# Kernel optimization log

Measured on AMD Instinct MI355X. Metric: run time of the kernel, lower is better.

Reference implementation:

```python
import jax, jax.numpy as jnp
import numpy as np

VOCAB, CTX, EMBED, HEADS = 32000, 2048, 1024, 16


def setup_inputs() -> dict:
    key = jax.random.key(0)
    ks = jax.random.split(key, 10)
    E = EMBED
    s = 0.02
    return {
        "x": jax.random.randint(ks[0], (2, 2048), 0, VOCAB, dtype=jnp.int32),
        "tok_emb": jax.random.normal(ks[1], (VOCAB, E), jnp.float32) * s,
        "pos_emb": jax.random.normal(ks[2], (CTX, E), jnp.float32) * s,
        "qkv_w": jax.random.normal(ks[3], (E, 3 * E), jnp.float32) * s,
        "qkv_b": jnp.zeros((3 * E,), jnp.float32),
        "proj_w": jax.random.normal(ks[4], (E, E), jnp.float32) * s,
        "proj_b": jnp.zeros((E,), jnp.float32),
        "fc_w": jax.random.normal(ks[5], (E, VOCAB), jnp.float32) * s,
        "fc_b": jnp.zeros((VOCAB,), jnp.float32),
    }


def reference(x, tok_emb, pos_emb, qkv_w, qkv_b, proj_w, proj_b, fc_w, fc_b):
    B, T = x.shape
    H = HEADS
    E = tok_emb.shape[1]
    hd = E // H
    h = tok_emb[x] + pos_emb[:T][None, :, :]                      # [B,T,E]
    qkv = h @ qkv_w + qkv_b                                       # [B,T,3E]
    q, k, v = jnp.split(qkv, 3, axis=-1)
    # [B,T,E] -> [B,H,T,hd]
    q = q.reshape(B, T, H, hd).transpose(0, 2, 1, 3)
    k = k.reshape(B, T, H, hd).transpose(0, 2, 1, 3)
    v = v.reshape(B, T, H, hd).transpose(0, 2, 1, 3)
    att = jnp.einsum("bhqd,bhkd->bhqk", q, k) / jnp.sqrt(jnp.float32(hd))
    causal = jnp.tril(jnp.ones((T, T), dtype=bool))
    att = jnp.where(causal[None, None], att, jnp.float32(-jnp.inf))
    att = jax.nn.softmax(att, axis=-1)
    out = jnp.einsum("bhqk,bhkd->bhqd", att, v)                   # [B,H,T,hd]
    out = out.transpose(0, 2, 1, 3).reshape(B, T, E)
    out = out @ proj_w + proj_b
    return out @ fc_w + fc_b                                      # [B,T,VOCAB]
```

## Files before the change

### kernel.cpp

```cpp
#include <hip/hip_runtime.h>

#define BATCH 2
#define T 2048
#define E 1024
#define NH 16
#define HD 64
#define M (BATCH*T)
#define K3 (3*E)
#define VOCAB 32000

typedef __attribute__((ext_vector_type(8))) short s16x8;
typedef __attribute__((ext_vector_type(4))) short s16x4;
typedef __attribute__((ext_vector_type(4))) float f32x4;

__device__ inline unsigned short f2bf(float f) {
  union { float f; unsigned u; } x; x.f = f;
  unsigned r = x.u + 0x7fffu + ((x.u >> 16) & 1u);
  return (unsigned short)(r >> 16);
}

__device__ inline void gload16(const void* g, void* l) {
  __builtin_amdgcn_global_load_lds(
      (const __attribute__((address_space(1))) unsigned int*)g,
      (__attribute__((address_space(3))) unsigned int*)l, 16, 0, 0);
}

__device__ inline void wt_body(const float* __restrict__ W,
    unsigned short* __restrict__ Wt, int N, int n0, int k0, int t,
    float (*tile)[65]) {
  int kl = t >> 2, c = t & 3;
  #pragma unroll
  for (int i = 0; i < 4; i++) {
    float4 v4 = *(const float4*)(W + (size_t)(k0 + kl) * N + n0 + c * 16 + i * 4);
    tile[kl][c * 16 + i * 4 + 0] = v4.x;
    tile[kl][c * 16 + i * 4 + 1] = v4.y;
    tile[kl][c * 16 + i * 4 + 2] = v4.z;
    tile[kl][c * 16 + i * 4 + 3] = v4.w;
  }
  __syncthreads();
  #pragma unroll
  for (int j = 0; j < 2; j++) {
    int idx = t + j * 256;
    int nl = idx >> 3, kq = (idx & 7) * 8;
    s16x8 o;
    #pragma unroll
    for (int i = 0; i < 8; i++) o[i] = (short)f2bf(tile[kq + i][nl]);
    *(s16x8*)(Wt + (size_t)(n0 + nl) * 1024 + k0 + kq) = o;
  }
}

__global__ __launch_bounds__(256) void k_pre(const int* __restrict__ x,
    const float* __restrict__ tok, const float* __restrict__ pos,
    unsigned short* __restrict__ hb,
    const float* __restrict__ qkvw, unsigned short* __restrict__ qkvwt,
    const float* __restrict__ projw, unsigned short* __restrict__ projwt) {
  __shared__ __align__(16) float tile[64][65];
  int gid = blockIdx.x, t = threadIdx.x;
  if (gid < 4096) {
    int row = gid;
    int tt = row & (T - 1);
    int tokid = x[row];
    float4 a = ((const float4*)(tok + (size_t)tokid * E))[t];
    float4 p = ((const float4*)(pos + (size_t)tt * E))[t];
    s16x4 o;
    o[0] = (short)f2bf(a.x + p.x); o[1] = (short)f2bf(a.y + p.y);
    o[2] = (short)f2bf(a.z + p.z); o[3] = (short)f2bf(a.w + p.w);
    *(s16x4*)(hb + (size_t)row * E + t * 4) = o;
    return;
  }
  if (gid < 4864) {
    int idx = gid - 4096;
    wt_body(qkvw, qkvwt, K3, (idx % 48) * 64, (idx / 48) * 64, t, tile);
    return;
  }
  int idx = gid - 4864;
  wt_body(projw, projwt, E, (idx % 16) * 64, (idx / 16) * 64, t, tile);
}

template<int MODE>
__global__ __launch_bounds__(256) void k_bgemm(
    const unsigned short* __restrict__ A, const unsigned short* __restrict__ Bt,
    const float* __restrict__ bias, float* __restrict__ C, int N,
    unsigned short* __restrict__ qo, unsigned short* __restrict__ ko,
    unsigned short* __restrict__ vo, unsigned short* __restrict__ Cb) {
  __shared__ char lds[16384];
  char* As = lds;
  char* Bs = lds + 8192;
  int tid = threadIdx.x;
  int lane = tid & 63;
  int wv = tid >> 6;
  int wm = wv >> 1, wn = wv & 1;
  int n0 = blockIdx.x * 128, m0 = blockIdx.y * 128;
  int fr = lane & 15, fq = lane >> 4;

  f32x4 acc[4][4];
  #pragma unroll
  for (int i = 0; i < 4; i++)
    #pragma unroll
    for (int j = 0; j < 4; j++) acc[i][j] = (f32x4){0.f, 0.f, 0.f, 0.f};

  int p0 = tid * 16, p1 = tid * 16 + 4096;
  int r0 = p0 >> 6, c0 = p0 & 63;
  int r1 = p1 >> 6, c1 = p1 & 63;
  int cs0 = c0 ^ (((r0 >> 1) & 3) << 4);
  int cs1 = c1 ^ (((r1 >> 1) & 3) << 4);
  const char* ga0 = (const char*)(A + (size_t)(m0 + r0) * 1024) + cs0;
  const char* ga1 = (const char*)(A + (size_t)(m0 + r1) * 1024) + cs1;
  const char* gb0 = (const char*)(Bt + (size_t)(n0 + r0) * 1024) + cs0;
  const char* gb1 = (const char*)(Bt + (size_t)(n0 + r1) * 1024) + cs1;

  int aoff[4], boff[4];
  #pragma unroll
  for (int i = 0; i < 4; i++) {
    int ra = wm * 64 + i * 16 + fr;
    aoff[i] = ra * 64 + ((fq * 16) ^ (((ra >> 1) & 3) << 4));
    int rb = wn * 64 + i * 16 + fr;
    boff[i] = rb * 64 + ((fq * 16) ^ (((rb >> 1) & 3) << 4));
  }

  for (int kb = 0; kb < 2048; kb += 64) {
    gload16(ga0 + kb, As + p0);
    gload16(ga1 + kb, As + p1);
    gload16(gb0 + kb, Bs + p0);
    gload16(gb1 + kb, Bs + p1);
    __syncthreads();
    s16x8 af[4], bfr[4];
    #pragma unroll
    for (int i = 0; i < 4; i++) af[i] = *(const s16x8*)(As + aoff[i]);
    #pragma unroll
    for (int i = 0; i < 4; i++) bfr[i] = *(const s16x8*)(Bs + boff[i]);
    #pragma unroll
    for (int mi = 0; mi < 4; mi++)
      #pragma unroll
      for (int ni = 0; ni < 4; ni++)
        acc[mi][ni] = __builtin_amdgcn_mfma_f32_16x16x32_bf16(
            af[mi], bfr[ni], acc[mi][ni], 0, 0, 0);
    __syncthreads();
  }

  if (MODE == 1) {
    #pragma unroll
    for (int mi = 0; mi < 4; mi++) {
      #pragma unroll
      for (int ni = 0; ni < 4; ni++) {
        int n = n0 + wn * 64 + ni * 16 + fr;
        int which = n >> 10;
        int e = n & (E - 1);
        int hh = e >> 6, d = e & 63;
        int mb = m0 + wm * 64 + mi * 16 + fq * 4;
        int b = mb >> 11, tt0 = mb & (T - 1);
        float bv = bias[n];
        if (which == 2) {
          s16x4 pk;
          #pragma unroll
          for (int j = 0; j < 4; j++) pk[j] = (short)f2bf(acc[mi][ni][j] + bv);
          *(s16x4*)(vo + ((size_t)(b * NH + hh) * 64 + d) * T + tt0) = pk;
        } else {
          unsigned short* dst = (which == 0) ? qo : ko;
          #pragma unroll
          for (int j = 0; j < 4; j++)
            dst[((size_t)(b * NH + hh) * T + tt0 + j) * 64 + d] =
                f2bf(acc[mi][ni][j] + bv);
        }
      }
    }
  } else {
    #pragma unroll
    for (int mi = 0; mi < 4; mi++) {
      #pragma unroll
      for (int ni = 0; ni < 4; ni++) {
        #pragma unroll
        for (int j = 0; j < 4; j++) {
          int m = m0 + wm * 64 + mi * 16 + fq * 4 + j;
          int n = n0 + wn * 64 + ni * 16 + fr;
          float val = acc[mi][ni][j] + bias[n];
          if (MODE == 0) C[(size_t)m * N + n] = val;
          else           Cb[(size_t)m * 1024 + n] = f2bf(val);
        }
      }
    }
  }
}

__global__ __launch_bounds__(512, 2) void k_fc(
    const unsigned short* __restrict__ A, const unsigned short* __restrict__ Bt,
    const float* __restrict__ bias, float* __restrict__ C) {
  __shared__ __align__(16) char lds[131072];
  int tid = threadIdx.x, lane = tid & 63, wv = tid >> 6;
  int WM = wv >> 2, WN = wv & 3;
  int fr = lane & 15, fq = lane >> 4;

  int bid = blockIdx.x;
  int wg = (bid & 7) * 250 + (bid >> 3);
  int m0 = (wg & 15) * 256;
  int n0 = (wg >> 4) * 256;

  const char* gA[4]; const char* gB[4]; int lo[4];
  #pragma unroll
  for (int j = 0; j < 4; j++) {
    int i = tid + j * 512;
    int r = i >> 3, c = i & 7;
    int cc = c ^ (r & 7);
    gA[j] = (const char*)A + ((size_t)(m0 + r) * 1024 + cc * 8) * 2;
    gB[j] = (const char*)Bt + ((size_t)(n0 + r) * 1024 + cc * 8) * 2;
    lo[j] = i * 16;
  }

  f32x4 acc[8][4];
  #pragma unroll
  for (int i = 0; i < 8; i++)
    #pragma unroll
    for (int j = 0; j < 4; j++) acc[i][j] = (f32x4){0.f, 0.f, 0.f, 0.f};

  #pragma unroll
  for (int j = 0; j < 4; j++) {
    gload16(gA[j], lds + lo[j]);
    gload16(gB[j], lds + 65536 + lo[j]);
  }
  __syncthreads();

  for (int t = 0; t < 16; t++) {
    int cur = t & 1;
    if (t + 1 < 16) {
      int kb = (t + 1) * 128;
      int nxt = cur ^ 1;
      #pragma unroll
      for (int j = 0; j < 4; j++) {
        gload16(gA[j] + kb, lds + nxt * 32768 + lo[j]);
        gload16(gB[j] + kb, lds + 65536 + nxt * 32768 + lo[j]);
      }
    }
    const char* As = lds + cur * 32768;
    const char* Bs = lds + 65536 + cur * 32768;
    #pragma unroll
    for (int kh = 0; kh < 2; kh++) {
      s16x8 af[8], bf[4];
      #pragma unroll
      for (int mi = 0; mi < 8; mi++) {
        int r = WM * 128 + mi * 16 + fr;
        af[mi] = *(const s16x8*)(As + r * 128 + (((kh * 4 + fq) ^ (r & 7)) << 4));
      }
      #pragma unroll
      for (int ni = 0; ni < 4; ni++) {
        int r = WN * 64 + ni * 16 + fr;
        bf[ni] = *(const s16x8*)(Bs + r * 128 + (((kh * 4 + fq) ^ (r & 7)) << 4));
      }
      __builtin_amdgcn_s_setprio(1);
      #pragma unroll
      for (int mi = 0; mi < 8; mi++)
        #pragma unroll
        for (int ni = 0; ni < 4; ni++)
          acc[mi][ni] = __builtin_amdgcn_mfma_f32_16x16x32_bf16(
              af[mi], bf[ni], acc[mi][ni], 0, 0, 0);
      __builtin_amdgcn_s_setprio(0);
    }
    __syncthreads();
  }

  #pragma unroll
  for (int mi = 0; mi < 8; mi++) {
    #pragma unroll
    for (int ni = 0; ni < 4; ni++) {
      int n = n0 + WN * 64 + ni * 16 + fr;
      float bv = bias[n];
      #pragma unroll
      for (int j = 0; j < 4; j++) {
        int m = m0 + WM * 128 + mi * 16 + fq * 4 + j;
        C[(size_t)m * VOCAB + n] = acc[mi][ni][j] + bv;
      }
    }
  }
}

#define BM 128
#define BN 128
#define BKF 32
#define LDT (BM + 4)
__global__ __launch_bounds__(256) void k_gemm32(
    const float* __restrict__ A, const float* __restrict__ Bw,
    const float* __restrict__ bias, float* __restrict__ C, int N) {
  __shared__ float As[BKF * LDT];
  __shared__ float Bs[BKF * LDT];
  int tid = threadIdx.x;
  int tx = tid & 15, ty = tid >> 4;
  int n0 = blockIdx.x * BN;
  int m0 = blockIdx.y * BM;
  float acc[8][8];
  #pragma unroll
  for (int i = 0; i < 8; i++)
    #pragma unroll
    for (int j = 0; j < 8; j++) acc[i][j] = 0.f;
  for (int k0 = 0; k0 < E; k0 += BKF) {
    #pragma unroll
    for (int i = 0; i < 4; i++) {
      int f = i * 256 + tid;
      int ml = f >> 3, c4 = f & 7;
      float4 va = *(const float4*)(A + (size_t)(m0 + ml) * E + k0 + c4 * 4);
      As[(c4 * 4 + 0) * LDT + ml] = va.x;
      As[(c4 * 4 + 1) * LDT + ml] = va.y;
      As[(c4 * 4 + 2) * LDT + ml] = va.z;
      As[(c4 * 4 + 3) * LDT + ml] = va.w;
    }
    #pragma unroll
    for (int i = 0; i < 4; i++) {
      int f = i * 256 + tid;
      int kk = f >> 5, c4 = f & 31;
      float4 vb = *(const float4*)(Bw + (size_t)(k0 + kk) * N + n0 + c4 * 4);
      *(float4*)(Bs + kk * LDT + c4 * 4) = vb;
    }
    __syncthreads();
    #pragma unroll
    for (int kk = 0; kk < BKF; kk++) {
      const float4* ar = (const float4*)(As + kk * LDT);
      const float4* br = (const float4*)(Bs + kk * LDT);
      float4 a0 = ar[ty * 2], a1 = ar[ty * 2 + 1];
      float4 b0 = br[tx * 2], b1 = br[tx * 2 + 1];
      float av[8] = {a0.x, a0.y, a0.z, a0.w, a1.x, a1.y, a1.z, a1.w};
      float bvv[8] = {b0.x, b0.y, b0.z, b0.w, b1.x, b1.y, b1.z, b1.w};
      #pragma unroll
      for (int i = 0; i < 8; i++)
        #pragma unroll
        for (int j = 0; j < 8; j++)
          acc[i][j] = fmaf(av[i], bvv[j], acc[i][j]);
    }
    __syncthreads();
  }
  int mbase = m0 + ty * 8;
  int nbase = n0 + tx * 8;
  #pragma unroll
  for (int i = 0; i < 8; i++) {
    float* crow = C + (size_t)(mbase + i) * N + nbase;
    #pragma unroll
    for (int j = 0; j < 8; j++) crow[j] = acc[i][j] + bias[nbase + j];
  }
}

__global__ __launch_bounds__(256) void k_attn_wt(
    const unsigned short* __restrict__ qb, const unsigned short* __restrict__ kb,
    const unsigned short* __restrict__ vtb, unsigned short* __restrict__ o,
    const float* __restrict__ fcw, unsigned short* __restrict__ fcwt) {
  __shared__ __align__(16) char lds[49152];
  int gid = blockIdx.x;
  int tid = threadIdx.x;

  if (gid >= 512) {
    int idx = gid - 512;
    wt_body(fcw, fcwt, VOCAB, (idx % 500) * 64, (idx / 500) * 64, tid,
            (float(*)[65])lds);
    return;
  }

  int qt = 15 - (gid >> 5);
  int bh = gid & 31;
  int b = bh >> 4, hh = bh & 15;
  int lane = tid & 63, wv = tid >> 6;
  int fr = lane & 15, fq = lane >> 4;
  int q0 = qt * 128;
  int qw0 = q0 + wv * 32;
  const char* Kg = (const char*)(kb + (size_t)bh * T * 64);
  const char* Vg = (const char*)(vtb + (size_t)bh * 64 * T);
  char* Pl = lds + 32768 + wv * 4096;

  s16x8 qf[2][2];
  #pragma unroll
  for (int g = 0; g < 2; g++) {
    const unsigned short* Qg = qb + ((size_t)bh * T + qw0 + g * 16) * 64;
    qf[g][0] = *(const s16x8*)(Qg + (size_t)fr * 64 + fq * 8);
    qf[g][1] = *(const s16x8*)(Qg + (size_t)fr * 64 + 32 + fq * 8);
  }

  f32x4 po[2][4];
  float mrow[2][4], lrow[2][4];
  #pragma unroll
  for (int g = 0; g < 2; g++)
    #pragma unroll
    for (int j = 0; j < 4; j++) {
      po[g][j] = (f32x4){0.f, 0.f, 0.f, 0.f};
      mrow[g][j] = -1e30f; lrow[g][j] = 0.f;
    }

  int ntiles = qt * 2 + 2;
  int i0 = tid, i1 = tid + 256;
  int sr0 = i0 >> 3, sc0 = ((i0 & 7) ^ (sr0 & 7)) << 4;
  int sr1 = i1 >> 3, sc1 = ((i1 & 7) ^ (sr1 & 7)) << 4;

  {
    gload16(Kg + (size_t)sr0 * 128 + sc0, lds + i0 * 16);
    gload16(Kg + (size_t)sr1 * 128 + sc1, lds + i1 * 16);
    gload16(Vg + (size_t)sr0 * (T * 2) + sc0, lds + 16384 + i0 * 16);
    gload16(Vg + (size_t)sr1 * (T * 2) + sc1, lds + 16384 + i1 * 16);
  }
  __syncthreads();
  int cur = 0;

  for (int kt = 0; kt < ntiles; kt++) {
    int kv0 = kt * 64;
    if (kt + 1 < ntiles) {
      size_t kvn = (size_t)(kv0 + 64);
      char* kd = lds + (cur ^ 1) * 8192;
      char* vd = lds + 16384 + (cur ^ 1) * 8192;
      gload16(Kg + (kvn + sr0) * 128 + sc0, kd + i0 * 16);
      gload16(Kg + (kvn + sr1) * 128 + sc1, kd + i1 * 16);
      gload16(Vg + (size_t)sr0 * (T * 2) + kvn * 2 + sc0, vd + i0 * 16);
      gload16(Vg + (size_t)sr1 * (T * 2) + kvn * 2 + sc1, vd + i1 * 16);
    }
    const char* Kt = lds + cur * 8192;
    const char* Vt = lds + 16384 + cur * 8192;

    f32x4 s[2][4];
    #pragma unroll
    for (int ni = 0; ni < 4; ni++) {
      int r = ni * 16 + fr;
      s16x8 kf0 = *(const s16x8*)(Kt + r * 128 + ((fq ^ (r & 7)) << 4));
      s16x8 kf1 = *(const s16x8*)(Kt + r * 128 + (((4 + fq) ^ (r & 7)) << 4));
      #pragma unroll
      for (int g = 0; g < 2; g++) {
        s[g][ni] = (f32x4){0.f, 0.f, 0.f, 0.f};
        s[g][ni] = __builtin_amdgcn_mfma_f32_16x16x32_bf16(qf[g][0], kf0, s[g][ni], 0, 0, 0);
        s[g][ni] = __builtin_amdgcn_mfma_f32_16x16x32_bf16(qf[g][1], kf1, s[g][ni], 0, 0, 0);
      }
    }

    #pragma unroll
    for (int g = 0; g < 2; g++) {
      int qw = qw0 + g * 16;
      bool needm = (kv0 + 63 > qw);
      #pragma unroll
      for (int jj = 0; jj < 4; jj++) {
        int row = qw + fq * 4 + jj;
        float tm = -1e30f;
        #pragma unroll
        for (int ni = 0; ni < 4; ni++) {
          float val = s[g][ni][jj] * 0.125f;
          if (needm) { int col = kv0 + ni * 16 + fr; if (col > row) val = -1e30f; }
          s[g][ni][jj] = val;
          tm = fmaxf(tm, val);
        }
        #pragma unroll
        for (int mk = 1; mk < 16; mk <<= 1) tm = fmaxf(tm, __shfl_xor(tm, mk));
        if (__any(tm > mrow[g][jj] + 8.f)) {
          float nm = fmaxf(mrow[g][jj], tm);
          float corr = __expf(mrow[g][jj] - nm);
          mrow[g][jj] = nm;
          #pragma unroll
          for (int ni = 0; ni < 4; ni++) po[g][ni][jj] *= corr;
          lrow[g][jj] *= corr;
        }
        float mref = mrow[g][jj];
        float rs = 0.f;
        #pragma unroll
        for (int ni = 0; ni < 4; ni++) {
          float pv = __expf(s[g][ni][jj] - mref);
          s[g][ni][jj] = pv;
          rs += pv;
        }
        #pragma unroll
        for (int mk = 1; mk < 16; mk <<= 1) rs += __shfl_xor(rs, mk);
        lrow[g][jj] += rs;
      }
    }

    asm volatile("s_waitcnt lgkmcnt(0)" ::: "memory");
    #pragma unroll
    for (int g = 0; g < 2; g++) {
      char* Pg = Pl + g * 2048;
      #pragma unroll
      for (int ni = 0; ni < 4; ni++) {
        int col = ni * 16 + fr;
        #pragma unroll
        for (int jj = 0; jj < 4; jj++) {
          int qq = fq * 4 + jj;
          *(unsigned short*)(Pg + qq * 128 + (((col >> 3) ^ (qq & 7)) << 4) +
                             (col & 7) * 2) = f2bf(s[g][ni][jj]);
        }
      }
    }
    asm volatile("s_waitcnt lgkmcnt(0)" ::: "memory");

    s16x8 pa[2][2];
    #pragma unroll
    for (int g = 0; g < 2; g++) {
      const char* Pg = Pl + g * 2048;
      pa[g][0] = *(const s16x8*)(Pg + fr * 128 + ((fq ^ (fr & 7)) << 4));
      pa[g][1] = *(const s16x8*)(Pg + fr * 128 + (((4 + fq) ^ (fr & 7)) << 4));
    }
    #pragma unroll
    for (int ni = 0; ni < 4; ni++) {
      int r = ni * 16 + fr;
      s16x8 vf0 = *(const s16x8*)(Vt + r * 128 + ((fq ^ (r & 7)) << 4));
      s16x8 vf1 = *(const s16x8*)(Vt + r * 128 + (((4 + fq) ^ (r & 7)) << 4));
      #pragma unroll
      for (int g = 0; g < 2; g++) {
        po[g][ni] = __builtin_amdgcn_mfma_f32_16x16x32_bf16(pa[g][0], vf0, po[g][ni], 0, 0, 0);
        po[g][ni] = __builtin_amdgcn_mfma_f32_16x16x32_bf16(pa[g][1], vf1, po[g][ni], 0, 0, 0);
      }
    }
    __syncthreads();
    cur ^= 1;
  }

  #pragma unroll
  for (int g = 0; g < 2; g++)
    #pragma unroll
    for (int jj = 0; jj < 4; jj++) {
      float inv = 1.f / lrow[g][jj];
      int row = qw0 + g * 16 + fq * 4 + jj;
      unsigned short* orow = o + ((size_t)(b * T + row)) * E + hh * 64;
      #pragma unroll
      for (int ni = 0; ni < 4; ni++)
        orow[ni * 16 + fr] = f2bf(po[g][ni][jj] * inv);
    }
}

extern "C" void kernel_launch(void* const* d_in, const int* in_sizes, int n_in,
                              void* d_out, int out_size, void* d_ws, size_t ws_size,
                              hipStream_t stream) {
  const int*   x      = (const int*)d_in[0];
  const float* tok    = (const float*)d_in[1];
  const float* pos    = (const float*)d_in[2];
  const float* qkv_w  = (const float*)d_in[3];
  const float* qkv_b  = (const float*)d_in[4];
  const float* proj_w = (const float*)d_in[5];
  const float* proj_b = (const float*)d_in[6];
  const float* fc_w   = (const float*)d_in[7];
  const float* fc_b   = (const float*)d_in[8];
  float* out = (float*)d_out;
  float* ws  = (float*)d_ws;

  unsigned short* hb      = (unsigned short*)out;
  unsigned short* qkv_wt  = (unsigned short*)(out + 2097152);
  unsigned short* qbuf    = (unsigned short*)(out + 3670016);
  unsigned short* kbuf    = (unsigned short*)(out + 5767168);
  unsigned short* vtbuf   = (unsigned short*)(out + 7864320);
  unsigned short* aob     = (unsigned short*)(out + 9961472);
  unsigned short* proj_wt = (unsigned short*)(out + 12058624);

  const size_t WS_FAST = (size_t)(2097152 + 16384000) * 4;

  k_pre<<<5120, 256, 0, stream>>>(x, tok, pos, hb, qkv_w, qkv_wt, proj_w, proj_wt);
  k_bgemm<1><<<dim3(K3 / 128, M / 128), 256, 0, stream>>>(
      hb, qkv_wt, qkv_b, nullptr, K3, qbuf, kbuf, vtbuf, nullptr);

  if (ws_size >= WS_FAST) {
    unsigned short* h2b   = (unsigned short*)ws;
    unsigned short* fc_wt = (unsigned short*)(ws + 2097152);
    k_attn_wt<<<8512, 256, 0, stream>>>(qbuf, kbuf, vtbuf, aob, fc_w, fc_wt);
    k_bgemm<2><<<dim3(E / 128, M / 128), 256, 0, stream>>>(
        aob, proj_wt, proj_b, nullptr, E, nullptr, nullptr, nullptr, h2b);
    k_fc<<<dim3((M / 256) * (VOCAB / 256)), 512, 0, stream>>>(
        h2b, fc_wt, fc_b, out);
  } else {
    float* h2 = ws;
    k_attn_wt<<<512, 256, 0, stream>>>(qbuf, kbuf, vtbuf, aob, nullptr, nullptr);
    k_bgemm<0><<<dim3(E / 128, M / 128), 256, 0, stream>>>(
        aob, proj_wt, proj_b, h2, E, nullptr, nullptr, nullptr, nullptr);
    k_gemm32<<<dim3(VOCAB / BN, M / BM), 256, 0, stream>>>(
        h2, fc_w, fc_b, out, VOCAB);
  }
}
```

Baseline: 512.9 us.

## Replace QKV projection GEMM with large-tile double-buffered swizzled-LDS kernel

The QKV projection moves from the generic 128x128 k_bgemm to a dedicated k_qkv kernel. It uses 256x256 tiles, 512 threads, and 128 KB of LDS with double-buffered K=128 stages and XOR-swizzled LDS layout. It also raises wave priority around MFMA bursts and remaps block indices to improve L2 locality. This is meant to raise data reuse per load and overlap global loads with MFMA compute. The cost is only 192 blocks, which may underfill the GPU's compute units.

Result: faster. 501.7 us (-2.2%).

```diff
diff --git a/kernel.cpp b/kernel.cpp
--- a/kernel.cpp
+++ b/kernel.cpp
@@ -81,8 +81,7 @@
 __global__ __launch_bounds__(256) void k_bgemm(
     const unsigned short* __restrict__ A, const unsigned short* __restrict__ Bt,
     const float* __restrict__ bias, float* __restrict__ C, int N,
-    unsigned short* __restrict__ qo, unsigned short* __restrict__ ko,
-    unsigned short* __restrict__ vo, unsigned short* __restrict__ Cb) {
+    unsigned short* __restrict__ Cb) {
   __shared__ char lds[16384];
   char* As = lds;
   char* Bs = lds + 8192;
@@ -138,45 +137,121 @@
     __syncthreads();
   }
 
-  if (MODE == 1) {
-    #pragma unroll
-    for (int mi = 0; mi < 4; mi++) {
+  #pragma unroll
+  for (int mi = 0; mi < 4; mi++) {
+    #pragma unroll
+    for (int ni = 0; ni < 4; ni++) {
+      #pragma unroll
+      for (int j = 0; j < 4; j++) {
+        int m = m0 + wm * 64 + mi * 16 + fq * 4 + j;
+        int n = n0 + wn * 64 + ni * 16 + fr;
+        float val = acc[mi][ni][j] + bias[n];
+        if (MODE == 0) C[(size_t)m * N + n] = val;
+        else           Cb[(size_t)m * 1024 + n] = f2bf(val);
+      }
+    }
+  }
+}
+
+__global__ __launch_bounds__(512, 2) void k_qkv(
+    const unsigned short* __restrict__ A, const unsigned short* __restrict__ Bt,
+    const float* __restrict__ bias,
+    unsigned short* __restrict__ qo, unsigned short* __restrict__ ko,
+    unsigned short* __restrict__ vo) {
+  __shared__ __align__(16) char lds[131072];
+  int tid = threadIdx.x, lane = tid & 63, wv = tid >> 6;
+  int WM = wv >> 2, WN = wv & 3;
+  int fr = lane & 15, fq = lane >> 4;
+
+  int bid = blockIdx.x;
+  int wg = (bid & 7) * 24 + (bid >> 3);
+  int m0 = (wg % 16) * 256;
+  int n0 = (wg / 16) * 256;
+
+  const char* gA[4]; const char* gB[4]; int lo[4];
+  #pragma unroll
+  for (int j = 0; j < 4; j++) {
+    int i = tid + j * 512;
+    int r = i >> 3, c = i & 7;
+    int cc = c ^ (r & 7);
+    gA[j] = (const char*)A + ((size_t)(m0 + r) * 1024 + cc * 8) * 2;
+    gB[j] = (const char*)Bt + ((size_t)(n0 + r) * 1024 + cc * 8) * 2;
+    lo[j] = i * 16;
+  }
+
+  f32x4 acc[8][4];
+  #pragma unroll
+  for (int i = 0; i < 8; i++)
+    #pragma unroll
+    for (int j = 0; j < 4; j++) acc[i][j] = (f32x4){0.f, 0.f, 0.f, 0.f};
+
+  #pragma unroll
+  for (int j = 0; j < 4; j++) {
+    gload16(gA[j], lds + lo[j]);
+    gload16(gB[j], lds + 65536 + lo[j]);
+  }
+  __syncthreads();
+
+  for (int t = 0; t < 16; t++) {
+    int cur = t & 1;
+    if (t + 1 < 16) {
+      int kb = (t + 1) * 128;
+      int nxt = cur ^ 1;
+      #pragma unroll
+      for (int j = 0; j < 4; j++) {
+        gload16(gA[j] + kb, lds + nxt * 32768 + lo[j]);
+        gload16(gB[j] + kb, lds + 65536 + nxt * 32768 + lo[j]);
+      }
+    }
+    const char* As = lds + cur * 32768;
+    const char* Bs = lds + 65536 + cur * 32768;
+    #pragma unroll
+    for (int kh = 0; kh < 2; kh++) {
+      s16x8 af[8], bf[4];
+      #pragma unroll
+      for (int mi = 0; mi < 8; mi++) {
+        int r = WM * 128 + mi * 16 + fr;
+        af[mi] = *(const s16x8*)(As + r * 128 + (((kh * 4 + fq) ^ (r & 7)) << 4));
+      }
       #pragma unroll
       for (int ni = 0; ni < 4; ni++) {
-        int n = n0 + wn * 64 + ni * 16 + fr;
-        int which = n >> 10;
-        int e = n & (E - 1);
-        int hh = e >> 6, d = e & 63;
-        int mb = m0 + wm * 64 + mi * 16 + fq * 4;
-        int b = mb >> 11, tt0 = mb & (T - 1);
-        float bv = bias[n];
-        if (which == 2) {
-          s16x4 pk;
-          #pragma unroll
-          for (int j = 0; j < 4; j++) pk[j] = (short)f2bf(acc[mi][ni][j] + bv);
-          *(s16x4*)(vo + ((size_t)(b * NH + hh) * 64 + d) * T + tt0) = pk;
-        } else {
-          unsigned short* dst = (which == 0) ? qo : ko;
-          #pragma unroll
-          for (int j = 0; j < 4; j++)
-            dst[((size_t)(b * NH + hh) * T + tt0 + j) * 64 + d] =
-                f2bf(acc[mi][ni][j] + bv);
-        }
-      }
-    }
-  } else {
-    #pragma unroll
-    for (int mi = 0; mi < 4; mi++) {
-      #pragma unroll
-      for (int ni = 0; ni < 4; ni++) {
-        #pragma unroll
-        for (int j = 0; j < 4; j++) {
-          int m = m0 + wm * 64 + mi * 16 + fq * 4 + j;
-          int n = n0 + wn * 64 + ni * 16 + fr;
-          float val = acc[mi][ni][j] + bias[n];
-          if (MODE == 0) C[(size_t)m * N + n] = val;
-          else           Cb[(size_t)m * 1024 + n] = f2bf(val);
-        }
+        int r = WN * 64 + ni * 16 + fr;
+        bf[ni] = *(const s16x8*)(Bs + r * 128 + (((kh * 4 + fq) ^ (r & 7)) << 4));
+      }
+      __builtin_amdgcn_s_setprio(1);
+      #pragma unroll
+      for (int mi = 0; mi < 8; mi++)
+        #pragma unroll
+        for (int ni = 0; ni < 4; ni++)
+          acc[mi][ni] = __builtin_amdgcn_mfma_f32_16x16x32_bf16(
+              af[mi], bf[ni], acc[mi][ni], 0, 0, 0);
+      __builtin_amdgcn_s_setprio(0);
+    }
+    __syncthreads();
+  }
+
+  #pragma unroll
+  for (int mi = 0; mi < 8; mi++) {
+    #pragma unroll
+    for (int ni = 0; ni < 4; ni++) {
+      int n = n0 + WN * 64 + ni * 16 + fr;
+      int which = n >> 10;
+      int e = n & (E - 1);
+      int hh = e >> 6, d = e & 63;
+      int mb = m0 + WM * 128 + mi * 16 + fq * 4;
+      int b = mb >> 11, tt0 = mb & (T - 1);
+      float bv = bias[n];
+      if (which == 2) {
+        s16x4 pk;
+        #pragma unroll
+        for (int j = 0; j < 4; j++) pk[j] = (short)f2bf(acc[mi][ni][j] + bv);
+        *(s16x4*)(vo + ((size_t)(b * NH + hh) * 64 + d) * T + tt0) = pk;
+      } else {
+        unsigned short* dst = (which == 0) ? qo : ko;
+        #pragma unroll
+        for (int j = 0; j < 4; j++)
+          dst[((size_t)(b * NH + hh) * T + tt0 + j) * 64 + d] =
+              f2bf(acc[mi][ni][j] + bv);
       }
     }
   }
@@ -538,22 +613,21 @@
   const size_t WS_FAST = (size_t)(2097152 + 16384000) * 4;
 
   k_pre<<<5120, 256, 0, stream>>>(x, tok, pos, hb, qkv_w, qkv_wt, proj_w, proj_wt);
-  k_bgemm<1><<<dim3(K3 / 128, M / 128), 256, 0, stream>>>(
-      hb, qkv_wt, qkv_b, nullptr, K3, qbuf, kbuf, vtbuf, nullptr);
+  k_qkv<<<192, 512, 0, stream>>>(hb, qkv_wt, qkv_b, qbuf, kbuf, vtbuf);
 
   if (ws_size >= WS_FAST) {
     unsigned short* h2b   = (unsigned short*)ws;
     unsigned short* fc_wt = (unsigned short*)(ws + 2097152);
     k_attn_wt<<<8512, 256, 0, stream>>>(qbuf, kbuf, vtbuf, aob, fc_w, fc_wt);
     k_bgemm<2><<<dim3(E / 128, M / 128), 256, 0, stream>>>(
-        aob, proj_wt, proj_b, nullptr, E, nullptr, nullptr, nullptr, h2b);
+        aob, proj_wt, proj_b, nullptr, E, h2b);
     k_fc<<<dim3((M / 256) * (VOCAB / 256)), 512, 0, stream>>>(
         h2b, fc_wt, fc_b, out);
   } else {
     float* h2 = ws;
     k_attn_wt<<<512, 256, 0, stream>>>(qbuf, kbuf, vtbuf, aob, nullptr, nullptr);
     k_bgemm<0><<<dim3(E / 128, M / 128), 256, 0, stream>>>(
-        aob, proj_wt, proj_b, h2, E, nullptr, nullptr, nullptr, nullptr);
+        aob, proj_wt, proj_b, h2, E, nullptr);
     k_gemm32<<<dim3(VOCAB / BN, M / BM), 256, 0, stream>>>(
         h2, fc_w, fc_b, out, VOCAB);
   }
```
